# Performance work log

Measured on AMD Instinct MI355X. Metric: run time of the kernel, lower is better.

The kernel has to match this reference:

```python
import jax, jax.numpy as jnp
import numpy as np
from functools import partial

B, INPUT_DIM, CHUNK, D, NLAYERS, FF, NCLS = 16, 20480, 10, 256, 4, 1024, 10
L = INPUT_DIM // CHUNK  # 2048
FILT_EMB, FILT_HID = 16, 64
EPS = 1e-5


def sinusoidal_pe(length, dim):
    pos = jnp.arange(length, dtype=jnp.float32)[:, None]
    div = jnp.exp(jnp.arange(0, dim, 2, dtype=jnp.float32) * (-np.log(10000.0) / dim))
    ang = pos * div  # (length, dim//2)
    pe = jnp.zeros((length, dim), dtype=jnp.float32)
    pe = pe.at[:, 0::2].set(jnp.sin(ang)).at[:, 1::2].set(jnp.cos(ang))
    return pe


def layernorm(x, g, b):
    mu = jnp.mean(x, axis=-1, keepdims=True)
    var = jnp.mean(jnp.square(x - mu), axis=-1, keepdims=True)
    return (x - mu) * jax.lax.rsqrt(var + EPS) * g + b


def setup_inputs() -> dict:
    key = jax.random.key(0)
    ks = iter(jax.random.split(key, 32))
    s = 0.02
    r = lambda shape: jax.random.normal(next(ks), shape, dtype=jnp.float32) * s
    inp = {
        'x': jax.random.normal(next(ks), (B, INPUT_DIM), dtype=jnp.float32),
        'inp_w': r((CHUNK, D)), 'inp_b': jnp.zeros((D,)),
        'in_proj_w': r((NLAYERS, D, 3 * D)), 'in_proj_b': jnp.zeros((NLAYERS, 3 * D)),
        'short_w': r((NLAYERS, D, 3)), 'short_b': jnp.zeros((NLAYERS, D)),
        'filt_w1': r((NLAYERS, FILT_EMB, FILT_HID)), 'filt_b1': jnp.zeros((NLAYERS, FILT_HID)),
        'filt_w2': r((NLAYERS, FILT_HID, D)), 'filt_b2': jnp.zeros((NLAYERS, D)),
        'out_w': r((NLAYERS, D, D)), 'out_b': jnp.zeros((NLAYERS, D)),
        'ln1_g': jnp.ones((NLAYERS, D)), 'ln1_b': jnp.zeros((NLAYERS, D)),
        'ln2_g': jnp.ones((NLAYERS, D)), 'ln2_b': jnp.zeros((NLAYERS, D)),
        'ffn_w1': r((NLAYERS, D, FF)), 'ffn_b1': jnp.zeros((NLAYERS, FF)),
        'ffn_w2': r((NLAYERS, FF, D)), 'ffn_b2': jnp.zeros((NLAYERS, D)),
        'norm_g': jnp.ones((D,)), 'norm_b': jnp.zeros((D,)),
        'cls_w': r((D, NCLS)), 'cls_b': jnp.zeros((NCLS,)),
    }
    return inp


def _hyena_op(u, in_w, in_b, sw, sb, fw1, fb1, fw2, fb2, ow, ob, pe16):
    # u: (B, L, D)
    proj = u @ in_w + in_b                       # (B, L, 3D)
    x0, x1, x2 = jnp.split(proj, 3, axis=-1)
    # depthwise short conv, kernel 3, same padding
    x0t = jnp.transpose(x0, (0, 2, 1))           # (B, D, L)
    x0c = jax.lax.conv_general_dilated(
        x0t, sw[:, None, :], window_strides=(1,), padding=[(1, 1)],
        feature_group_count=D, dimension_numbers=('NCH', 'OIH', 'NCH'))
    x0c = jnp.transpose(x0c + sb[None, :, None], (0, 2, 1))  # (B, L, D)
    # implicit long filter from positional MLP
    h = jax.nn.gelu(pe16 @ fw1 + fb1, approximate=False) @ fw2 + fb2  # (L, D)
    # FFT causal-style long conv (n = 2L)
    xf = jnp.fft.rfft(x0c, n=2 * L, axis=1)
    hf = jnp.fft.rfft(h, n=2 * L, axis=0)
    y = jnp.fft.irfft(xf * hf[None], n=2 * L, axis=1)[:, :L, :]
    y = y * x1 * x2                              # elementwise gating
    return y @ ow + ob


def reference(x, inp_w, inp_b, in_proj_w, in_proj_b, short_w, short_b,
              filt_w1, filt_b1, filt_w2, filt_b2, out_w, out_b,
              ln1_g, ln1_b, ln2_g, ln2_b, ffn_w1, ffn_b1, ffn_w2, ffn_b2,
              norm_g, norm_b, cls_w, cls_b):
    xs = x.reshape(B, L, CHUNK) @ inp_w + inp_b  # (B, L, D)
    xs = xs + sinusoidal_pe(L, D)[None]
    pe16 = sinusoidal_pe(L, FILT_EMB)
    for i in range(NLAYERS):
        h = _hyena_op(layernorm(xs, ln1_g[i], ln1_b[i]),
                      in_proj_w[i], in_proj_b[i], short_w[i], short_b[i],
                      filt_w1[i], filt_b1[i], filt_w2[i], filt_b2[i],
                      out_w[i], out_b[i], pe16)
        xs = xs + h
        z = layernorm(xs, ln2_g[i], ln2_b[i])
        z = jax.nn.gelu(z @ ffn_w1[i] + ffn_b1[i], approximate=False) @ ffn_w2[i] + ffn_b2[i]
        xs = xs + z
    pooled = layernorm(jnp.mean(xs, axis=1), norm_g, norm_b)
    return pooled @ cls_w + cls_b
```

## Files before the change

kernel.cpp:

```cpp
#include <hip/hip_runtime.h>
#include <math.h>

#define BB 16
#define LL 2048
#define CHUNK 10
#define DD 256
#define NLAYERS 4
#define FFD 1024
#define NCLS 10
#define HSTRC 2056

typedef short bf16x8 __attribute__((ext_vector_type(8)));
typedef short s16x4 __attribute__((ext_vector_type(4)));
typedef float f32x4 __attribute__((ext_vector_type(4)));

__device__ __forceinline__ unsigned short f2bf(float f) {
    unsigned int u = __builtin_bit_cast(unsigned int, f);
    u = (u + 0x7FFF + ((u >> 16) & 1)) >> 16;
    return (unsigned short)u;
}
__device__ __forceinline__ float bf2f(unsigned short s) {
    unsigned int u = ((unsigned int)s) << 16;
    return __builtin_bit_cast(float, u);
}
__device__ __forceinline__ float bfLO(unsigned v) { return __builtin_bit_cast(float, v << 16); }
__device__ __forceinline__ float bfHI(unsigned v) { return __builtin_bit_cast(float, v & 0xFFFF0000u); }

#define PADC(a) ((a) + ((a) >> 4))

__device__ __forceinline__ float2 cmulf(float2 a, float2 b) {
    return make_float2(fmaf(-a.y, b.y, a.x * b.x), fmaf(a.y, b.x, a.x * b.y));
}

#define GLL16(gsrc, ldst) \
    __builtin_amdgcn_global_load_lds((const __attribute__((address_space(1))) void*)(gsrc), \
                                     (__attribute__((address_space(3))) void*)(ldst), 16, 0, 0)

__global__ __launch_bounds__(256)
void embed_k(const float* __restrict__ x, const float* __restrict__ iw,
             const float* __restrict__ ib, float* __restrict__ xs)
{
    const int tid = threadIdx.x;
    const size_t row0 = (size_t)blockIdx.x * 8;
    const int i2 = (tid >> 1) * 2;
    const float div = expf(-0.03597789207803197f * (float)i2);
    float wcol[CHUNK];
#pragma unroll
    for (int c = 0; c < CHUNK; ++c) wcol[c] = iw[c * DD + tid];
    const float bv = ib[tid];
    for (int rr = 0; rr < 8; ++rr) {
        size_t row = row0 + rr;
        int l = (int)(row & (LL - 1));
        const float* xr = x + row * CHUNK;
        float acc = bv;
#pragma unroll
        for (int c = 0; c < CHUNK; ++c) acc += xr[c] * wcol[c];
        float sv, cv;
        sincosf((float)l * div, &sv, &cv);
        acc += (tid & 1) ? cv : sv;
        xs[row * DD + tid] = acc;
    }
}

__global__ __launch_bounds__(256)
void filt_k(const float* __restrict__ fw1, const float* __restrict__ fb1,
            const float* __restrict__ fw2, const float* __restrict__ fb2,
            float* __restrict__ hT)
{
    __shared__ float pe[16];
    __shared__ float hid[64];
    const int tid = threadIdx.x, l = blockIdx.x;
    if (tid < 16) {
        int i2 = (tid >> 1) * 2;
        float div = expf(-0.5756462732485114f * (float)i2);
        float sv, cv;
        sincosf((float)l * div, &sv, &cv);
        pe[tid] = (tid & 1) ? cv : sv;
    }
    __syncthreads();
    if (tid < 64) {
        float a = fb1[tid];
#pragma unroll
        for (int e = 0; e < 16; ++e) a += pe[e] * fw1[e * 64 + tid];
        hid[tid] = 0.5f * a * (1.0f + erff(a * 0.70710678118f));
    }
    __syncthreads();
    float a = fb2[tid];
#pragma unroll
    for (int h = 0; h < 64; ++h) a += hid[h] * fw2[h * DD + tid];
    hT[(size_t)tid * LL + l] = a;
}

__device__ __forceinline__ void dft4c(float2 a, float2 b, float2 c, float2 d,
                                      float2& F0, float2& F1, float2& F2, float2& F3)
{
    float t0r = a.x + c.x, t0i = a.y + c.y;
    float t1r = a.x - c.x, t1i = a.y - c.y;
    float t2r = b.x + d.x, t2i = b.y + d.y;
    float t3r = b.x - d.x, t3i = b.y - d.y;
    F0 = make_float2(t0r + t2r, t0i + t2i);
    F2 = make_float2(t0r - t2r, t0i - t2i);
    F1 = make_float2(t1r + t3i, t1i - t3r);
    F3 = make_float2(t1r - t3i, t1i + t3r);
}

template <int SH>
__device__ __forceinline__ void stage8(const float2* __restrict__ src,
                                       float2* __restrict__ dst, int tid)
{
    constexpr int ST = 1 << SH;
    __syncthreads();
    const int p = tid >> SH;
    const int q = tid & (ST - 1);
    float2 x0 = src[PADC(tid)];
    float2 x1 = src[PADC(tid + 256)];
    float2 x2 = src[PADC(tid + 512)];
    float2 x3 = src[PADC(tid + 768)];
    float2 x4 = src[PADC(tid + 1024)];
    float2 x5 = src[PADC(tid + 1280)];
    float2 x6 = src[PADC(tid + 1536)];
    float2 x7 = src[PADC(tid + 1792)];
    float2 E0, E1, E2, E3, O0, O1, O2, O3;
    dft4c(x0, x2, x4, x6, E0, E1, E2, E3);
    dft4c(x1, x3, x5, x7, O0, O1, O2, O3);
    const float C8 = 0.70710678118654752f;
    float2 y0 = make_float2(E0.x + O0.x, E0.y + O0.y);
    float2 y4 = make_float2(E0.x - O0.x, E0.y - O0.y);
    float a1 = C8 * (O1.x + O1.y), b1 = C8 * (O1.y - O1.x);
    float2 y1 = make_float2(E1.x + a1, E1.y + b1);
    float2 y5 = make_float2(E1.x - a1, E1.y - b1);
    float2 y2 = make_float2(E2.x + O2.y, E2.y - O2.x);
    float2 y6 = make_float2(E2.x - O2.y, E2.y + O2.x);
    float a3 = -C8 * (O3.x - O3.y), b3 = -C8 * (O3.x + O3.y);
    float2 y3 = make_float2(E3.x + a3, E3.y + b3);
    float2 y7 = make_float2(E3.x - a3, E3.y - b3);
    const int k0 = p << SH;
    float s1, c1;
    __sincosf(-3.0679615757712823e-3f * (float)k0, &s1, &c1);
    float2 w1 = make_float2(c1, s1);
    float2 w2 = cmulf(w1, w1);
    float2 w3 = cmulf(w2, w1);
    float2 w4 = cmulf(w2, w2);
    float2 w5 = cmulf(w3, w2);
    float2 w6 = cmulf(w3, w3);
    float2 w7 = cmulf(w4, w3);
    const int ob = q + ((ST * p) << 3);
    dst[PADC(ob)] = y0;
    dst[PADC(ob + ST)] = cmulf(w1, y1);
    dst[PADC(ob + 2 * ST)] = cmulf(w2, y2);
    dst[PADC(ob + 3 * ST)] = cmulf(w3, y3);
    dst[PADC(ob + 4 * ST)] = cmulf(w4, y4);
    dst[PADC(ob + 5 * ST)] = cmulf(w5, y5);
    dst[PADC(ob + 6 * ST)] = cmulf(w6, y6);
    dst[PADC(ob + 7 * ST)] = cmulf(w7, y7);
}

__device__ __forceinline__ void stage4f(const float2* __restrict__ src,
                                        float2* __restrict__ dst, int tid)
{
    __syncthreads();
#pragma unroll
    for (int jj = 0; jj < 2; ++jj) {
        int u = tid + (jj << 8);
        float2 a = src[PADC(u)], b = src[PADC(u + 512)];
        float2 c = src[PADC(u + 1024)], d = src[PADC(u + 1536)];
        float2 F0, F1, F2, F3;
        dft4c(a, b, c, d, F0, F1, F2, F3);
        dst[PADC(u)] = F0;
        dst[PADC(u + 512)] = F1;
        dst[PADC(u + 1024)] = F2;
        dst[PADC(u + 1536)] = F3;
    }
}

__device__ __forceinline__ void fft2048c(float2* __restrict__ A, float2* __restrict__ B, int tid)
{
    stage8<0>(A, B, tid);
    stage8<3>(B, A, tid);
    stage8<6>(A, B, tid);
    stage4f(B, A, tid);
    __syncthreads();
}

__global__ __launch_bounds__(256)
void ffth_k(const float* __restrict__ hT, float2* __restrict__ Hf)
{
    __shared__ float2 A2[2176], B2[2176];
    const int tid = threadIdx.x, d = blockIdx.x;
    const float2* rowf = reinterpret_cast<const float2*>(hT + (size_t)d * LL);
#pragma unroll
    for (int j = 0; j < 4; ++j) {
        int u = tid + (j << 8);
        A2[PADC(u)] = rowf[u];
        A2[PADC(u + 1024)] = make_float2(0.0f, 0.0f);
    }
    fft2048c(A2, B2, tid);
    float2* hf = Hf + (size_t)d * HSTRC;
#pragma unroll
    for (int j = 0; j < 4; ++j) {
        int k = 1 + tid + (j << 8);
        int m = 2048 - k;
        float2 zk = A2[PADC(k)], zm = A2[PADC(m)];
        float Er = 0.5f * (zk.x + zm.x), Ei = 0.5f * (zk.y - zm.y);
        float Or = 0.5f * (zk.y + zm.y), Oi = -0.5f * (zk.x - zm.x);
        float ts, tc;
        __sincosf(-1.5339807878856412e-3f * (float)k, &ts, &tc);
        float TOr = tc * Or - ts * Oi, TOi = tc * Oi + ts * Or;
        hf[k] = make_float2(Er + TOr, Ei + TOi);
        hf[m] = make_float2(Er - TOr, -(Ei - TOi));
    }
    if (tid == 0) {
        float2 z0 = A2[PADC(0)];
        hf[0] = make_float2(z0.x + z0.y, z0.x - z0.y);
    }
}

__global__ __launch_bounds__(256)
void fftconv_k(const unsigned short* __restrict__ x0T, unsigned short* __restrict__ yT,
               const float2* __restrict__ Hf, const float* __restrict__ sw,
               const float* __restrict__ sb)
{
    __shared__ float2 A2[2176], B2[2176];
    const int tid = threadIdx.x;
    const int w = blockIdx.x;
    const int c = w & 7, s = w >> 3;
    const int d = c * 32 + (s & 31);
    const int b = s >> 5;
    const int blk = b * 256 + d;
    const float w0 = sw[d * 3], w1 = sw[d * 3 + 1], w2 = sw[d * 3 + 2];
    const float bv = sb[d];

    float* rawF = reinterpret_cast<float*>(B2);
    {
        const uint4* rowv = reinterpret_cast<const uint4*>(x0T + (size_t)blk * LL);
        uint4 ld = rowv[tid];
        int p = tid << 3;
        int lB = p & ~63;
        int p6 = p & 63;
        int fg = p6 >> 4;
        int m0 = (p6 >> 2) & 3;
        float4* d0 = reinterpret_cast<float4*>(rawF + lB + m0 * 16 + fg * 4);
        float4* d1 = reinterpret_cast<float4*>(rawF + lB + (m0 + 1) * 16 + fg * 4);
        *d0 = make_float4(bfLO(ld.x), bfHI(ld.x), bfLO(ld.y), bfHI(ld.y));
        *d1 = make_float4(bfLO(ld.z), bfHI(ld.z), bfLO(ld.w), bfHI(ld.w));
    }
    __syncthreads();
#pragma unroll
    for (int j = 0; j < 4; ++j) {
        int u = tid + (j << 8);
        float xm1 = (u == 0) ? 0.0f : rawF[2 * u - 1];
        float xc0 = rawF[2 * u];
        float xp1 = rawF[2 * u + 1];
        float xp2 = (u == 1023) ? 0.0f : rawF[2 * u + 2];
        float e = bv + w0 * xm1 + w1 * xc0 + w2 * xp1;
        float o = bv + w0 * xc0 + w1 * xp1 + w2 * xp2;
        A2[PADC(u)] = make_float2(e, o);
        A2[PADC(u + 1024)] = make_float2(0.0f, 0.0f);
    }
    fft2048c(A2, B2, tid);
    const float2* hf = Hf + (size_t)d * HSTRC;
#pragma unroll
    for (int j = 0; j < 4; ++j) {
        int k = 1 + tid + (j << 8);
        int m = 2048 - k;
        float2 zk = A2[PADC(k)], zm = A2[PADC(m)];
        float Er = 0.5f * (zk.x + zm.x), Ei = 0.5f * (zk.y - zm.y);
        float Or = 0.5f * (zk.y + zm.y), Oi = -0.5f * (zk.x - zm.x);
        float ts, tc;
        __sincosf(-1.5339807878856412e-3f * (float)k, &ts, &tc);
        float TOr = tc * Or - ts * Oi, TOi = tc * Oi + ts * Or;
        float Xpr = Er + TOr, Xpi = Ei + TOi;
        float Xmr = Er - TOr, Xmi = Ei - TOi;
        float2 hk = hf[k], hm = hf[m];
        float Ykr = Xpr * hk.x - Xpi * hk.y, Yki = Xpr * hk.y + Xpi * hk.x;
        float Cr = Xmr * hm.x + Xmi * hm.y, Ci = Xmi * hm.x - Xmr * hm.y;
        float Pr = 0.5f * (Ykr + Cr), Pi = 0.5f * (Yki + Ci);
        float Gr = 0.5f * (Ykr - Cr), Gi = 0.5f * (Yki - Ci);
        float Qr = tc * Gr + ts * Gi, Qi = tc * Gi - ts * Gr;
        B2[PADC(k)] = make_float2(Pr - Qi, -(Pi + Qr));
        B2[PADC(m)] = make_float2(Pr + Qi, Pi - Qr);
    }
    if (tid == 0) {
        float2 z0 = A2[PADC(0)];
        float2 h0 = hf[0];
        float X0 = z0.x + z0.y, X2 = z0.x - z0.y;
        float Y0 = X0 * h0.x, Y2 = X2 * h0.y;
        float P = 0.5f * (Y0 + Y2), Q = 0.5f * (Y0 - Y2);
        B2[PADC(0)] = make_float2(P, -Q);
    }
    stage8<0>(B2, A2, tid);
    stage8<3>(A2, B2, tid);
    stage8<6>(B2, A2, tid);
    stage4f(A2, B2, tid);
    __syncthreads();
    const float sc = 1.0f / 2048.0f;
    unsigned* yrow = reinterpret_cast<unsigned*>(yT + (size_t)blk * LL);
#pragma unroll
    for (int j = 0; j < 4; ++j) {
        int u = tid + (j << 8);
        float2 v = B2[PADC(u)];
        float e = v.x * sc, o = -v.y * sc;
        yrow[u] = (unsigned)f2bf(e) | ((unsigned)f2bf(o) << 16);
    }
}

__global__ __launch_bounds__(256)
void gate_k(const unsigned short* __restrict__ yTb, const unsigned short* __restrict__ px,
            unsigned short* __restrict__ yg)
{
    __shared__ float t[64][65];
    const int tid = threadIdx.x;
    const int blk = blockIdx.x;
    const int b = blk >> 7;
    const int dt = (blk >> 5) & 3;
    const int lt = blk & 31;
    const int d0 = dt << 6, l0 = lt << 6;
    const int r0 = tid >> 6, c = tid & 63;
    for (int rr = 0; rr < 16; ++rr) {
        int dl = rr * 4 + r0;
        t[dl][c] = bf2f(yTb[(((size_t)(b << 8) + d0 + dl) << 11) + l0 + c]);
    }
    __syncthreads();
    const int lid = tid & 63, lr = tid >> 6;
    for (int k = 0; k < 16; ++k) {
        int ll = k * 4 + lr;
        int l = l0 + ll;
        size_t pb = ((size_t)(b * LL + l)) * 512;
        float v = t[lid][ll];
        float x1 = bf2f(px[pb + d0 + lid]);
        float x2 = bf2f(px[pb + 256 + d0 + lid]);
        yg[((size_t)(b * LL + l)) * DD + d0 + lid] = f2bf(v * x1 * x2);
    }
}

__global__ __launch_bounds__(256)
void lncast_k(const float* __restrict__ xs, const float* __restrict__ g,
              const float* __restrict__ b, unsigned short* __restrict__ o)
{
    const int tid = threadIdx.x, lane = tid & 63, wave = tid >> 6;
    const size_t row = (size_t)blockIdx.x * 4 + wave;
    float4 v = reinterpret_cast<const float4*>(xs + row * DD)[lane];
    float s = v.x + v.y + v.z + v.w;
#pragma unroll
    for (int off = 32; off > 0; off >>= 1) s += __shfl_xor(s, off, 64);
    float mean = s * (1.0f / 256.0f);
    float e0 = v.x - mean, e1 = v.y - mean, e2 = v.z - mean, e3 = v.w - mean;
    float q = e0 * e0 + e1 * e1 + e2 * e2 + e3 * e3;
#pragma unroll
    for (int off = 32; off > 0; off >>= 1) q += __shfl_xor(q, off, 64);
    float rstd = rsqrtf(q * (1.0f / 256.0f) + 1e-5f);
    float4 gg = reinterpret_cast<const float4*>(g)[lane];
    float4 bb = reinterpret_cast<const float4*>(b)[lane];
    s16x4 r;
    r[0] = (short)f2bf(e0 * rstd * gg.x + bb.x);
    r[1] = (short)f2bf(e1 * rstd * gg.y + bb.y);
    r[2] = (short)f2bf(e2 * rstd * gg.z + bb.z);
    r[3] = (short)f2bf(e3 * rstd * gg.w + bb.w);
    *reinterpret_cast<s16x4*>(o + row * DD + lane * 4) = r;
}

__global__ __launch_bounds__(256)
void wcastT_k(const float* __restrict__ W, unsigned short* __restrict__ WT, int K, int N)
{
    __shared__ float t[32][33];
    const int tx = threadIdx.x & 31, ty = threadIdx.x >> 5;
    const int n0 = blockIdx.x * 32, k0 = blockIdx.y * 32;
#pragma unroll
    for (int j = 0; j < 4; ++j)
        t[ty + 8 * j][tx] = W[(size_t)(k0 + ty + 8 * j) * N + n0 + tx];
    __syncthreads();
#pragma unroll
    for (int j = 0; j < 4; ++j)
        WT[(size_t)(n0 + ty + 8 * j) * K + k0 + tx] = f2bf(t[tx][ty + 8 * j]);
}

template <int K, int N, int MODE>
__global__ __launch_bounds__(256)
void gemm_k(const unsigned short* __restrict__ A, const unsigned short* __restrict__ WT,
            const float* __restrict__ bias, void* __restrict__ outp, void* __restrict__ outp2)
{
    constexpr int C = N / 128;
    __shared__ unsigned short ldsA[8192];
    __shared__ unsigned short ldsB[8192];
    const int tid = threadIdx.x;
    const int lane = tid & 63, wid = tid >> 6;
    const int nwg = gridDim.x;
    const int w = blockIdx.x;
    const int logical = (w & 7) * (nwg >> 3) + (w >> 3);
    const int row0 = (logical / C) * 128;
    const int col0 = (logical % C) * 128;
    const int wm = (wid >> 1) * 64, wn = (wid & 1) * 64;
    const int fr = lane & 15, fg = lane >> 4;

    f32x4 acc[4][4];
#pragma unroll
    for (int n = 0; n < 4; ++n) {
        float bv = bias[col0 + wn + n * 16 + fr];
#pragma unroll
        for (int m = 0; m < 4; ++m) {
            acc[m][n][0] = bv; acc[m][n][1] = bv; acc[m][n][2] = bv; acc[m][n][3] = bv;
        }
    }

    const int srow = wid * 8 + (lane >> 3);
    const int sc = lane & 7;

    for (int kt = 0; kt < K / 64; ++kt) {
        const int k0 = kt * 64;
#pragma unroll
        for (int it = 0; it < 4; ++it) {
            int row = it * 32 + srow;
            int cs = sc ^ (row & 7);
            const char* ga = (const char*)(A + (size_t)(row0 + row) * K + k0) + cs * 16;
            const char* gb = (const char*)(WT + (size_t)(col0 + row) * K + k0) + cs * 16;
            GLL16(ga, (char*)ldsA + it * 4096 + wid * 1024);
            GLL16(gb, (char*)ldsB + it * 4096 + wid * 1024);
        }
        __syncthreads();
#pragma unroll
        for (int ks = 0; ks < 2; ++ks) {
            bf16x8 af[4], bf[4];
#pragma unroll
            for (int m = 0; m < 4; ++m) {
                int ar = wm + m * 16 + fr;
                int slot = (ks * 4 + fg) ^ (ar & 7);
                af[m] = *reinterpret_cast<const bf16x8*>(ldsA + ar * 64 + slot * 8);
            }
#pragma unroll
            for (int n = 0; n < 4; ++n) {
                int br = wn + n * 16 + fr;
                int slot = (ks * 4 + fg) ^ (br & 7);
                bf[n] = *reinterpret_cast<const bf16x8*>(ldsB + br * 64 + slot * 8);
            }
#pragma unroll
            for (int m = 0; m < 4; ++m)
#pragma unroll
                for (int n = 0; n < 4; ++n)
                    acc[m][n] = __builtin_amdgcn_mfma_f32_16x16x32_bf16(af[m], bf[n], acc[m][n], 0, 0, 0);
        }
        __syncthreads();
    }

    if constexpr (MODE == 3) {
        if (col0 < 256) {
            const int b = row0 >> 11;
            const int lb0 = (row0 & (LL - 1)) + wm;
#pragma unroll
            for (int n = 0; n < 4; ++n) {
                int dcol = col0 + wn + n * 16 + fr;
                unsigned short* dst = (unsigned short*)outp +
                    (((size_t)(b << 8) + dcol) << 11) + lb0 + fg * 16;
                unsigned pk[8];
#pragma unroll
                for (int q = 0; q < 8; ++q) {
                    int m = q >> 1, r0 = (q & 1) * 2;
                    pk[q] = (unsigned)f2bf(acc[m][n][r0]) | ((unsigned)f2bf(acc[m][n][r0 + 1]) << 16);
                }
                *reinterpret_cast<uint4*>(dst)     = make_uint4(pk[0], pk[1], pk[2], pk[3]);
                *reinterpret_cast<uint4*>(dst + 8) = make_uint4(pk[4], pk[5], pk[6], pk[7]);
            }
        } else {
            unsigned short* px = (unsigned short*)outp2;
#pragma unroll
            for (int m = 0; m < 4; ++m) {
                int gr = row0 + wm + m * 16 + fg * 4;
#pragma unroll
                for (int n = 0; n < 4; ++n) {
                    int gc = col0 - 256 + wn + n * 16 + fr;
#pragma unroll
                    for (int r = 0; r < 4; ++r)
                        px[(size_t)(gr + r) * 512 + gc] = f2bf(acc[m][n][r]);
                }
            }
        }
        return;
    }

#pragma unroll
    for (int m = 0; m < 4; ++m) {
        int gr = row0 + wm + m * 16 + fg * 4;
#pragma unroll
        for (int n = 0; n < 4; ++n) {
            int gc = col0 + wn + n * 16 + fr;
#pragma unroll
            for (int r = 0; r < 4; ++r) {
                float v = acc[m][n][r];
                if constexpr (MODE == 1) v = 0.5f * v * (1.0f + erff(v * 0.70710678118f));
                if constexpr (MODE <= 1) {
                    ((unsigned short*)outp)[(size_t)(gr + r) * N + gc] = f2bf(v);
                } else {
                    float* o = (float*)outp + (size_t)(gr + r) * N + gc;
                    *o += v;
                }
            }
        }
    }
}

__global__ __launch_bounds__(256)
void pool_k(const float* __restrict__ xs, float* __restrict__ part)
{
    const int tid = threadIdx.x;
    const int b = blockIdx.x >> 4, g = blockIdx.x & 15;
    size_t base = ((size_t)b * LL + g * 128) * DD + tid;
    float s = 0.0f;
    for (int l = 0; l < 128; ++l) s += xs[base + (size_t)l * DD];
    part[(size_t)blockIdx.x * DD + tid] = s;
}

__global__ __launch_bounds__(256)
void final_k(const float* __restrict__ part, const float* __restrict__ ng,
             const float* __restrict__ nb, const float* __restrict__ cw,
             const float* __restrict__ cb, float* __restrict__ out)
{
    __shared__ float pl[256];
    __shared__ float red[4], red2[4];
    const int tid = threadIdx.x, b = blockIdx.x;
    float m = 0.0f;
    for (int g = 0; g < 16; ++g) m += part[((size_t)b * 16 + g) * DD + tid];
    m *= (1.0f / (float)LL);
    const int lane = tid & 63, wave = tid >> 6;
    float s = m;
#pragma unroll
    for (int off = 32; off > 0; off >>= 1) s += __shfl_xor(s, off, 64);
    if (lane == 0) red[wave] = s;
    __syncthreads();
    float mean = (red[0] + red[1] + red[2] + red[3]) * (1.0f / 256.0f);
    float dm = m - mean;
    float qv = dm * dm;
#pragma unroll
    for (int off = 32; off > 0; off >>= 1) qv += __shfl_xor(qv, off, 64);
    if (lane == 0) red2[wave] = qv;
    __syncthreads();
    float var = (red2[0] + red2[1] + red2[2] + red2[3]) * (1.0f / 256.0f);
    pl[tid] = dm * rsqrtf(var + 1e-5f) * ng[tid] + nb[tid];
    __syncthreads();
    if (tid < NCLS) {
        float a = cb[tid];
        for (int dd = 0; dd < 256; ++dd) a += pl[dd] * cw[dd * NCLS + tid];
        out[b * NCLS + tid] = a;
    }
}

extern "C" void kernel_launch(void* const* d_in, const int* in_sizes, int n_in,
                              void* d_out, int out_size, void* d_ws, size_t ws_size,
                              hipStream_t stream)
{
    (void)in_sizes; (void)n_in; (void)out_size; (void)ws_size;
    const float* x        = (const float*)d_in[0];
    const float* inp_w    = (const float*)d_in[1];
    const float* inp_b    = (const float*)d_in[2];
    const float* in_proj_w= (const float*)d_in[3];
    const float* in_proj_b= (const float*)d_in[4];
    const float* short_w  = (const float*)d_in[5];
    const float* short_b  = (const float*)d_in[6];
    const float* filt_w1  = (const float*)d_in[7];
    const float* filt_b1  = (const float*)d_in[8];
    const float* filt_w2  = (const float*)d_in[9];
    const float* filt_b2  = (const float*)d_in[10];
    const float* out_w    = (const float*)d_in[11];
    const float* out_b    = (const float*)d_in[12];
    const float* ln1_g    = (const float*)d_in[13];
    const float* ln1_b    = (const float*)d_in[14];
    const float* ln2_g    = (const float*)d_in[15];
    const float* ln2_b    = (const float*)d_in[16];
    const float* ffn_w1   = (const float*)d_in[17];
    const float* ffn_b1   = (const float*)d_in[18];
    const float* ffn_w2   = (const float*)d_in[19];
    const float* ffn_b2   = (const float*)d_in[20];
    const float* norm_g   = (const float*)d_in[21];
    const float* norm_b   = (const float*)d_in[22];
    const float* cls_w    = (const float*)d_in[23];
    const float* cls_b    = (const float*)d_in[24];

    float* ws = (float*)d_ws;
    float* xs            = ws;
    unsigned short* xln  = (unsigned short*)(ws + 8388608);
    unsigned short* x0T  = (unsigned short*)(ws + 12582912);
    unsigned short* yT   = (unsigned short*)(ws + 16777216);
    unsigned short* projx= (unsigned short*)(ws + 20971520);
    unsigned short* ygp  = x0T;
    unsigned short* hid  = x0T;
    float* hT            = ws + 29360128;
    float2* Hf           = (float2*)(ws + 29884416);
    float* part          = ws + 30937088;
    unsigned short* WTb  = (unsigned short*)(ws + 31002624);

    for (int i = 0; i < NLAYERS; ++i) {
        unsigned short* wt = WTb + (size_t)i * 786432;
        wcastT_k<<<dim3(24, 8), 256, 0, stream>>>(in_proj_w + (size_t)i * 196608, wt, 256, 768);
        wcastT_k<<<dim3(8, 8), 256, 0, stream>>>(out_w + (size_t)i * 65536, wt + 196608, 256, 256);
        wcastT_k<<<dim3(32, 8), 256, 0, stream>>>(ffn_w1 + (size_t)i * 262144, wt + 262144, 256, 1024);
        wcastT_k<<<dim3(8, 32), 256, 0, stream>>>(ffn_w2 + (size_t)i * 262144, wt + 524288, 1024, 256);
    }

    embed_k<<<4096, 256, 0, stream>>>(x, inp_w, inp_b, xs);

    for (int i = 0; i < NLAYERS; ++i) {
        unsigned short* wt = WTb + (size_t)i * 786432;
        filt_k<<<LL, 256, 0, stream>>>(filt_w1 + i * 1024, filt_b1 + i * 64,
                                       filt_w2 + i * 16384, filt_b2 + i * 256, hT);
        ffth_k<<<DD, 256, 0, stream>>>(hT, Hf);
        lncast_k<<<8192, 256, 0, stream>>>(xs, ln1_g + i * 256, ln1_b + i * 256, xln);
        gemm_k<256, 768, 3><<<1536, 256, 0, stream>>>(
            xln, wt, in_proj_b + i * 768, x0T, projx);
        fftconv_k<<<4096, 256, 0, stream>>>(x0T, yT, Hf, short_w + i * 768, short_b + i * 256);
        gate_k<<<2048, 256, 0, stream>>>(yT, projx, ygp);
        gemm_k<256, 256, 2><<<512, 256, 0, stream>>>(
            ygp, wt + 196608, out_b + i * 256, xs, nullptr);
        lncast_k<<<8192, 256, 0, stream>>>(xs, ln2_g + i * 256, ln2_b + i * 256, xln);
        gemm_k<256, 1024, 1><<<2048, 256, 0, stream>>>(
            xln, wt + 262144, ffn_b1 + i * 1024, hid, nullptr);
        gemm_k<1024, 256, 2><<<512, 256, 0, stream>>>(
            hid, wt + 524288, ffn_b2 + i * 256, xs, nullptr);
    }

    pool_k<<<BB * 16, 256, 0, stream>>>(xs, part);
    final_k<<<BB, 256, 0, stream>>>(part, norm_g, norm_b, cls_w, cls_b, (float*)d_out);
}
```

Measured before the change: 789.0 us.

## Fuse LayerNorm into residual GEMM epilogues and run FFT in place

Adds a GEMM kernel whose 64-row tile covers the full 256-wide output. Its epilogue adds the residual, computes the LayerNorm row statistics with cross-lane shuffles, and writes both the updated fp32 residual and the bf16 normalized activations. This removes the separate lncast passes after the out-projection and FFN2 GEMMs. Separately, the FFT stages now run in place in a single shared-memory buffer with extra barriers, halving LDS use so more fftconv blocks can be resident (launch bounds set to 4). The trade-offs are extra synchronization, single-pass variance, and each GEMM block holding a wide accumulator tile.

```diff
diff --git a/kernel.cpp b/kernel.cpp
--- a/kernel.cpp
+++ b/kernel.cpp
@@ -105,21 +105,19 @@
 }
 
 template <int SH>
-__device__ __forceinline__ void stage8(const float2* __restrict__ src,
-                                       float2* __restrict__ dst, int tid)
+__device__ __forceinline__ void stage8ip(float2* __restrict__ A, int tid)
 {
     constexpr int ST = 1 << SH;
-    __syncthreads();
     const int p = tid >> SH;
     const int q = tid & (ST - 1);
-    float2 x0 = src[PADC(tid)];
-    float2 x1 = src[PADC(tid + 256)];
-    float2 x2 = src[PADC(tid + 512)];
-    float2 x3 = src[PADC(tid + 768)];
-    float2 x4 = src[PADC(tid + 1024)];
-    float2 x5 = src[PADC(tid + 1280)];
-    float2 x6 = src[PADC(tid + 1536)];
-    float2 x7 = src[PADC(tid + 1792)];
+    float2 x0 = A[PADC(tid)];
+    float2 x1 = A[PADC(tid + 256)];
+    float2 x2 = A[PADC(tid + 512)];
+    float2 x3 = A[PADC(tid + 768)];
+    float2 x4 = A[PADC(tid + 1024)];
+    float2 x5 = A[PADC(tid + 1280)];
+    float2 x6 = A[PADC(tid + 1536)];
+    float2 x7 = A[PADC(tid + 1792)];
     float2 E0, E1, E2, E3, O0, O1, O2, O3;
     dft4c(x0, x2, x4, x6, E0, E1, E2, E3);
     dft4c(x1, x3, x5, x7, O0, O1, O2, O3);
@@ -144,48 +142,63 @@
     float2 w5 = cmulf(w3, w2);
     float2 w6 = cmulf(w3, w3);
     float2 w7 = cmulf(w4, w3);
+    float2 o1 = cmulf(w1, y1);
+    float2 o2 = cmulf(w2, y2);
+    float2 o3 = cmulf(w3, y3);
+    float2 o4 = cmulf(w4, y4);
+    float2 o5 = cmulf(w5, y5);
+    float2 o6 = cmulf(w6, y6);
+    float2 o7 = cmulf(w7, y7);
+    __syncthreads();
     const int ob = q + ((ST * p) << 3);
-    dst[PADC(ob)] = y0;
-    dst[PADC(ob + ST)] = cmulf(w1, y1);
-    dst[PADC(ob + 2 * ST)] = cmulf(w2, y2);
-    dst[PADC(ob + 3 * ST)] = cmulf(w3, y3);
-    dst[PADC(ob + 4 * ST)] = cmulf(w4, y4);
-    dst[PADC(ob + 5 * ST)] = cmulf(w5, y5);
-    dst[PADC(ob + 6 * ST)] = cmulf(w6, y6);
-    dst[PADC(ob + 7 * ST)] = cmulf(w7, y7);
-}
-
-__device__ __forceinline__ void stage4f(const float2* __restrict__ src,
-                                        float2* __restrict__ dst, int tid)
-{
-    __syncthreads();
+    A[PADC(ob)] = y0;
+    A[PADC(ob + ST)] = o1;
+    A[PADC(ob + 2 * ST)] = o2;
+    A[PADC(ob + 3 * ST)] = o3;
+    A[PADC(ob + 4 * ST)] = o4;
+    A[PADC(ob + 5 * ST)] = o5;
+    A[PADC(ob + 6 * ST)] = o6;
+    A[PADC(ob + 7 * ST)] = o7;
+    __syncthreads();
+}
+
+__device__ __forceinline__ void stage4fip(float2* __restrict__ A, int tid)
+{
+    float2 v[2][4];
 #pragma unroll
     for (int jj = 0; jj < 2; ++jj) {
         int u = tid + (jj << 8);
-        float2 a = src[PADC(u)], b = src[PADC(u + 512)];
-        float2 c = src[PADC(u + 1024)], d = src[PADC(u + 1536)];
+        v[jj][0] = A[PADC(u)];
+        v[jj][1] = A[PADC(u + 512)];
+        v[jj][2] = A[PADC(u + 1024)];
+        v[jj][3] = A[PADC(u + 1536)];
+    }
+    __syncthreads();
+#pragma unroll
+    for (int jj = 0; jj < 2; ++jj) {
+        int u = tid + (jj << 8);
         float2 F0, F1, F2, F3;
-        dft4c(a, b, c, d, F0, F1, F2, F3);
-        dst[PADC(u)] = F0;
-        dst[PADC(u + 512)] = F1;
-        dst[PADC(u + 1024)] = F2;
-        dst[PADC(u + 1536)] = F3;
-    }
-}
-
-__device__ __forceinline__ void fft2048c(float2* __restrict__ A, float2* __restrict__ B, int tid)
-{
-    stage8<0>(A, B, tid);
-    stage8<3>(B, A, tid);
-    stage8<6>(A, B, tid);
-    stage4f(B, A, tid);
-    __syncthreads();
+        dft4c(v[jj][0], v[jj][1], v[jj][2], v[jj][3], F0, F1, F2, F3);
+        A[PADC(u)] = F0;
+        A[PADC(u + 512)] = F1;
+        A[PADC(u + 1024)] = F2;
+        A[PADC(u + 1536)] = F3;
+    }
+    __syncthreads();
+}
+
+__device__ __forceinline__ void fft2048ip(float2* __restrict__ A, int tid)
+{
+    stage8ip<0>(A, tid);
+    stage8ip<3>(A, tid);
+    stage8ip<6>(A, tid);
+    stage4fip(A, tid);
 }
 
 __global__ __launch_bounds__(256)
 void ffth_k(const float* __restrict__ hT, float2* __restrict__ Hf)
 {
-    __shared__ float2 A2[2176], B2[2176];
+    __shared__ float2 A2[2176];
     const int tid = threadIdx.x, d = blockIdx.x;
     const float2* rowf = reinterpret_cast<const float2*>(hT + (size_t)d * LL);
 #pragma unroll
@@ -194,7 +207,8 @@
         A2[PADC(u)] = rowf[u];
         A2[PADC(u + 1024)] = make_float2(0.0f, 0.0f);
     }
-    fft2048c(A2, B2, tid);
+    __syncthreads();
+    fft2048ip(A2, tid);
     float2* hf = Hf + (size_t)d * HSTRC;
 #pragma unroll
     for (int j = 0; j < 4; ++j) {
@@ -215,12 +229,12 @@
     }
 }
 
-__global__ __launch_bounds__(256)
+__global__ __launch_bounds__(256, 4)
 void fftconv_k(const unsigned short* __restrict__ x0T, unsigned short* __restrict__ yT,
                const float2* __restrict__ Hf, const float* __restrict__ sw,
                const float* __restrict__ sb)
 {
-    __shared__ float2 A2[2176], B2[2176];
+    __shared__ float2 A2[2176];
     const int tid = threadIdx.x;
     const int w = blockIdx.x;
     const int c = w & 7, s = w >> 3;
@@ -230,7 +244,7 @@
     const float w0 = sw[d * 3], w1 = sw[d * 3 + 1], w2 = sw[d * 3 + 2];
     const float bv = sb[d];
 
-    float* rawF = reinterpret_cast<float*>(B2);
+    float* rawF = reinterpret_cast<float*>(A2);
     {
         const uint4* rowv = reinterpret_cast<const uint4*>(x0T + (size_t)blk * LL);
         uint4 ld = rowv[tid];
@@ -245,6 +259,7 @@
         *d1 = make_float4(bfLO(ld.z), bfHI(ld.z), bfLO(ld.w), bfHI(ld.w));
     }
     __syncthreads();
+    float2 zv[4];
 #pragma unroll
     for (int j = 0; j < 4; ++j) {
         int u = tid + (j << 8);
@@ -252,12 +267,18 @@
         float xc0 = rawF[2 * u];
         float xp1 = rawF[2 * u + 1];
         float xp2 = (u == 1023) ? 0.0f : rawF[2 * u + 2];
-        float e = bv + w0 * xm1 + w1 * xc0 + w2 * xp1;
-        float o = bv + w0 * xc0 + w1 * xp1 + w2 * xp2;
-        A2[PADC(u)] = make_float2(e, o);
+        zv[j].x = bv + w0 * xm1 + w1 * xc0 + w2 * xp1;
+        zv[j].y = bv + w0 * xc0 + w1 * xp1 + w2 * xp2;
+    }
+    __syncthreads();
+#pragma unroll
+    for (int j = 0; j < 4; ++j) {
+        int u = tid + (j << 8);
+        A2[PADC(u)] = zv[j];
         A2[PADC(u + 1024)] = make_float2(0.0f, 0.0f);
     }
-    fft2048c(A2, B2, tid);
+    __syncthreads();
+    fft2048ip(A2, tid);
     const float2* hf = Hf + (size_t)d * HSTRC;
 #pragma unroll
     for (int j = 0; j < 4; ++j) {
@@ -277,8 +298,8 @@
         float Pr = 0.5f * (Ykr + Cr), Pi = 0.5f * (Yki + Ci);
         float Gr = 0.5f * (Ykr - Cr), Gi = 0.5f * (Yki - Ci);
         float Qr = tc * Gr + ts * Gi, Qi = tc * Gi - ts * Gr;
-        B2[PADC(k)] = make_float2(Pr - Qi, -(Pi + Qr));
-        B2[PADC(m)] = make_float2(Pr + Qi, Pi - Qr);
+        A2[PADC(k)] = make_float2(Pr - Qi, -(Pi + Qr));
+        A2[PADC(m)] = make_float2(Pr + Qi, Pi - Qr);
     }
     if (tid == 0) {
         float2 z0 = A2[PADC(0)];
@@ -286,19 +307,16 @@
         float X0 = z0.x + z0.y, X2 = z0.x - z0.y;
         float Y0 = X0 * h0.x, Y2 = X2 * h0.y;
         float P = 0.5f * (Y0 + Y2), Q = 0.5f * (Y0 - Y2);
-        B2[PADC(0)] = make_float2(P, -Q);
-    }
-    stage8<0>(B2, A2, tid);
-    stage8<3>(A2, B2, tid);
-    stage8<6>(B2, A2, tid);
-    stage4f(A2, B2, tid);
-    __syncthreads();
+        A2[PADC(0)] = make_float2(P, -Q);
+    }
+    __syncthreads();
+    fft2048ip(A2, tid);
     const float sc = 1.0f / 2048.0f;
     unsigned* yrow = reinterpret_cast<unsigned*>(yT + (size_t)blk * LL);
 #pragma unroll
     for (int j = 0; j < 4; ++j) {
         int u = tid + (j << 8);
-        float2 v = B2[PADC(u)];
+        float2 v = A2[PADC(u)];
         float e = v.x * sc, o = -v.y * sc;
         yrow[u] = (unsigned)f2bf(e) | ((unsigned)f2bf(o) << 16);
     }
@@ -493,6 +511,111 @@
                     *o += v;
                 }
             }
+        }
+    }
+}
+
+template <int K>
+__global__ __launch_bounds__(256)
+void gemm_ln_k(const unsigned short* __restrict__ A, const unsigned short* __restrict__ WT,
+               const float* __restrict__ bias, const float* __restrict__ lng,
+               const float* __restrict__ lnb, float* __restrict__ xs,
+               unsigned short* __restrict__ xln)
+{
+    __shared__ unsigned short ldsA[64 * 64];
+    __shared__ unsigned short ldsB[256 * 64];
+    const int tid = threadIdx.x;
+    const int lane = tid & 63, wid = tid >> 6;
+    const int nwg = gridDim.x;
+    const int w = blockIdx.x;
+    const int logical = (w & 7) * (nwg >> 3) + (w >> 3);
+    const size_t row0 = (size_t)logical * 64;
+    const int fr = lane & 15, fg = lane >> 4;
+
+    f32x4 acc[16];
+#pragma unroll
+    for (int n = 0; n < 16; ++n) {
+        float bv = bias[n * 16 + fr];
+        acc[n][0] = bv; acc[n][1] = bv; acc[n][2] = bv; acc[n][3] = bv;
+    }
+
+    for (int kt = 0; kt < K / 64; ++kt) {
+        const int k0 = kt * 64;
+#pragma unroll
+        for (int p = 0; p < 2; ++p) {
+            int cch = p * 256 + tid;
+            int row = cch >> 3;
+            int cs = (cch & 7) ^ (row & 7);
+            const char* ga = (const char*)(A + (row0 + row) * K + k0) + cs * 16;
+            GLL16(ga, (char*)ldsA + p * 4096 + wid * 1024);
+        }
+#pragma unroll
+        for (int p = 0; p < 8; ++p) {
+            int cch = p * 256 + tid;
+            int row = cch >> 3;
+            int cs = (cch & 7) ^ (row & 7);
+            const char* gb = (const char*)(WT + (size_t)row * K + k0) + cs * 16;
+            GLL16(gb, (char*)ldsB + p * 4096 + wid * 1024);
+        }
+        __syncthreads();
+#pragma unroll
+        for (int ks = 0; ks < 2; ++ks) {
+            int ar = wid * 16 + fr;
+            int slotA = (ks * 4 + fg) ^ (ar & 7);
+            bf16x8 af = *reinterpret_cast<const bf16x8*>(ldsA + ar * 64 + slotA * 8);
+#pragma unroll
+            for (int n = 0; n < 16; ++n) {
+                int br = n * 16 + fr;
+                int slotB = (ks * 4 + fg) ^ (br & 7);
+                bf16x8 bf = *reinterpret_cast<const bf16x8*>(ldsB + br * 64 + slotB * 8);
+                acc[n] = __builtin_amdgcn_mfma_f32_16x16x32_bf16(af, bf, acc[n], 0, 0, 0);
+            }
+        }
+        __syncthreads();
+    }
+
+    const size_t rbase = row0 + wid * 16 + fg * 4;
+#pragma unroll
+    for (int r = 0; r < 4; ++r) {
+        const float* xr = xs + (rbase + r) * DD;
+#pragma unroll
+        for (int n = 0; n < 16; ++n)
+            acc[n][r] += xr[fr + 16 * n];
+    }
+    float sm[4], sq[4];
+#pragma unroll
+    for (int r = 0; r < 4; ++r) {
+        float s = 0.0f, q = 0.0f;
+#pragma unroll
+        for (int n = 0; n < 16; ++n) {
+            float v = acc[n][r];
+            s += v; q += v * v;
+        }
+#pragma unroll
+        for (int off = 1; off < 16; off <<= 1) {
+            s += __shfl_xor(s, off, 64);
+            q += __shfl_xor(q, off, 64);
+        }
+        sm[r] = s * (1.0f / 256.0f);
+        float var = q * (1.0f / 256.0f) - sm[r] * sm[r];
+        sq[r] = rsqrtf(var + 1e-5f);
+    }
+    float gv[16], bvv[16];
+#pragma unroll
+    for (int n = 0; n < 16; ++n) {
+        gv[n] = lng[fr + 16 * n];
+        bvv[n] = lnb[fr + 16 * n];
+    }
+#pragma unroll
+    for (int r = 0; r < 4; ++r) {
+        float* xw = xs + (rbase + r) * DD;
+        unsigned short* lw = xln + (rbase + r) * DD;
+#pragma unroll
+        for (int n = 0; n < 16; ++n) {
+            int gc = fr + 16 * n;
+            float v = acc[n][r];
+            xw[gc] = v;
+            lw[gc] = f2bf((v - sm[r]) * sq[r] * gv[n] + bvv[n]);
         }
     }
 }
@@ -595,24 +718,29 @@
     }
 
     embed_k<<<4096, 256, 0, stream>>>(x, inp_w, inp_b, xs);
+    lncast_k<<<8192, 256, 0, stream>>>(xs, ln1_g, ln1_b, xln);
 
     for (int i = 0; i < NLAYERS; ++i) {
         unsigned short* wt = WTb + (size_t)i * 786432;
         filt_k<<<LL, 256, 0, stream>>>(filt_w1 + i * 1024, filt_b1 + i * 64,
                                        filt_w2 + i * 16384, filt_b2 + i * 256, hT);
         ffth_k<<<DD, 256, 0, stream>>>(hT, Hf);
-        lncast_k<<<8192, 256, 0, stream>>>(xs, ln1_g + i * 256, ln1_b + i * 256, xln);
         gemm_k<256, 768, 3><<<1536, 256, 0, stream>>>(
             xln, wt, in_proj_b + i * 768, x0T, projx);
         fftconv_k<<<4096, 256, 0, stream>>>(x0T, yT, Hf, short_w + i * 768, short_b + i * 256);
         gate_k<<<2048, 256, 0, stream>>>(yT, projx, ygp);
-        gemm_k<256, 256, 2><<<512, 256, 0, stream>>>(
-            ygp, wt + 196608, out_b + i * 256, xs, nullptr);
-        lncast_k<<<8192, 256, 0, stream>>>(xs, ln2_g + i * 256, ln2_b + i * 256, xln);
+        gemm_ln_k<256><<<512, 256, 0, stream>>>(
+            ygp, wt + 196608, out_b + i * 256, ln2_g + i * 256, ln2_b + i * 256, xs, xln);
         gemm_k<256, 1024, 1><<<2048, 256, 0, stream>>>(
             xln, wt + 262144, ffn_b1 + i * 1024, hid, nullptr);
-        gemm_k<1024, 256, 2><<<512, 256, 0, stream>>>(
-            hid, wt + 524288, ffn_b2 + i * 256, xs, nullptr);
+        if (i < NLAYERS - 1) {
+            gemm_ln_k<1024><<<512, 256, 0, stream>>>(
+                hid, wt + 524288, ffn_b2 + i * 256,
+                ln1_g + (i + 1) * 256, ln1_b + (i + 1) * 256, xs, xln);
+        } else {
+            gemm_k<1024, 256, 2><<<512, 256, 0, stream>>>(
+                hid, wt + 524288, ffn_b2 + i * 256, xs, nullptr);
+        }
     }
 
     pool_k<<<BB * 16, 256, 0, stream>>>(xs, part);
```

After: 788.1 us. About the same (-0.1%).
